# Optimization experiments

Hardware: AMD Instinct MI355X
Metric: run time of the kernel (lower is better)

Reference implementation:

```python
import jax, jax.numpy as jnp
import numpy as np

K = 1024          # num_embeddings
D = 768           # embedding_dim
COMMIT = 0.25     # commitment_cost
PW = 0.1          # perplexity_weight


def setup_inputs() -> dict:
    key = jax.random.key(0)
    k1, k2 = jax.random.split(key)
    inputs = jax.random.normal(k1, (32, 2048, D), dtype=jnp.float32)
    weight = jax.random.normal(k2, (K, D), dtype=jnp.float32)  # codebook
    return {"inputs": inputs, "weight": weight}


def reference(inputs, weight):
    """Eval-mode forward of VectorQuantizerEMA (deterministic nearest-code lookup)."""
    in_shape = inputs.shape
    flat = inputs.reshape(-1, D)                       # [N, D]
    valid = jnp.linalg.norm(flat, axis=1) > 1e-6       # padding mask [N]
    maskf = valid.astype(flat.dtype)
    n_valid = maskf.sum()

    dist = (jnp.sum(flat * flat, axis=1, keepdims=True)
            + jnp.sum(weight * weight, axis=1)
            - 2.0 * flat @ weight.T)

    idx = jnp.argmin(dist, axis=1)                     # [N]
    min_d = jnp.min(dist, axis=1)                      # [N]
    idx = jnp.where(valid, idx, 0)
    min_d = jnp.where(valid, min_d, 0.0)

    q_flat = weight[idx] * maskf[:, None]              # zeros at padded rows
    quantized = q_flat.reshape(in_shape)
    quantized_st = inputs + jax.lax.stop_gradient(quantized - inputs)

    # commitment loss: MSE over valid rows only
    sq_err = jnp.sum((flat - jax.lax.stop_gradient(q_flat)) ** 2, axis=1)
    loss_commit = jnp.sum(maskf * sq_err) / (n_valid * D)

    # perplexity over valid assignments (one-hot mean == normalized counts)
    counts = jnp.zeros((K,), flat.dtype).at[idx].add(maskf)
    avg_probs = counts / n_valid
    perplexity = jnp.exp(-jnp.sum(avg_probs * jnp.log(avg_probs + 1e-10)))
    perplexity_loss = -jnp.log(perplexity + 1e-10)

    total_loss = COMMIT * loss_commit + PW * perplexity_loss

    indices = idx.reshape(in_shape[:-1])
    min_distances = min_d.reshape(in_shape[:-1])
    return quantized_st, total_loss, indices, min_distances, perplexity
```

## Files before the change

kernel.cpp:

```cpp
#include <hip/hip_runtime.h>
#include <hip/hip_bf16.h>
#include <math.h>

#define NROWS 65536
#define DDIM  768
#define KCODES 1024
#define NCB   8
#define BM    128
#define BK    128
#define KC    32
#define NCH   (DDIM / KC)
#define BK2   32
#define NCH2  (DDIM / BK2)
#define GAP_TAU  0.3f
#define FILT_TAU 0.6f
#define RGRID 2048
#define QGRID 2048

#define OUT_LOSS ((size_t)NROWS * DDIM)
#define OUT_IDX  (OUT_LOSS + 1)
#define OUT_MIND (OUT_IDX + NROWS)
#define OUT_PERP (OUT_MIND + NROWS)

#define WS_SUM    0
#define WS_NSUS   8
#define WS_NVAL   12
#define WS_COUNTS 256
#define WS_WSQ    (WS_COUNTS + 4*KCODES)
#define WS_ROWS   (WS_WSQ + 4*KCODES)
#define WS_ROWI   (WS_ROWS + 4*NROWS)
#define WS_SUSP   (WS_ROWI + 4*NROWS)
#define WS_PM1    (WS_SUSP + 4*NROWS)
#define WS_PM2    (WS_PM1 + (size_t)4*NROWS*NCB)
#define WS_PIDX   (WS_PM2 + (size_t)4*NROWS*NCB)
#define WS_END    (WS_PIDX + (size_t)4*NROWS*NCB)
#define WS_AF16   ((WS_END + 255) & ~(size_t)255)
#define WS_WF16   (WS_AF16 + (size_t)NROWS * DDIM * 2)
#define WS_END2   (WS_WF16 + (size_t)KCODES * DDIM * 2)

typedef __attribute__((ext_vector_type(8))) _Float16 half8;
typedef __attribute__((ext_vector_type(4))) float f32x4;

#define GLOAD16(gsrc, ldst) \
    __builtin_amdgcn_global_load_lds( \
        (const __attribute__((address_space(1))) unsigned int*)(gsrc), \
        (__attribute__((address_space(3))) unsigned int*)(ldst), 16, 0, 0)

template <typename T>
__device__ inline T waveRedAdd(T v) {
#pragma unroll
    for (int o = 32; o; o >>= 1) v += __shfl_xor(v, o);
    return v;
}

__device__ inline ushort f2h(float f) {
    union { _Float16 h; ushort u; } c;
    c.h = (_Float16)f;
    return c.u;
}

__global__ void k_init(float* counts, int* n_suspect, unsigned* n_valid, double* sum_sqerr) {
    const int t = threadIdx.x;
    if (t == 0) { *n_suspect = 0; *n_valid = 0u; *sum_sqerr = 0.0; }
    for (int k = t; k < KCODES; k += 256) counts[k] = 0.f;
}

#define ASLOTS (NROWS * (DDIM / 8))
#define TSLOTS ((NROWS + KCODES) * (DDIM / 8))
__global__ __launch_bounds__(256) void k_convert(
    const float* __restrict__ A, const float* __restrict__ W,
    ushort* __restrict__ Af16, ushort* __restrict__ Wf16)
{
    for (int gidx = blockIdx.x * 256 + threadIdx.x; gidx < TSLOTS; gidx += gridDim.x * 256) {
        const float* src; ushort* dst; int sid;
        if (gidx < ASLOTS) { src = A; dst = Af16; sid = gidx; }
        else { src = W; dst = Wf16; sid = gidx - ASLOTS; }
        const int row = sid / 96;
        const int sl = sid - row * 96;
        const int ch = sl >> 2, s = sl & 3;
        const float* p = src + (size_t)row * DDIM + ch * 32 + s * 8;
        const float4 a = *(const float4*)p;
        const float4 b = *(const float4*)(p + 4);
        uint4 v;
        v.x = ((unsigned)f2h(a.y) << 16) | f2h(a.x);
        v.y = ((unsigned)f2h(a.w) << 16) | f2h(a.z);
        v.z = ((unsigned)f2h(b.y) << 16) | f2h(b.x);
        v.w = ((unsigned)f2h(b.w) << 16) | f2h(b.z);
        *(uint4*)(dst + (size_t)row * DDIM + ch * 32 + ((s ^ ((row >> 1) & 3)) << 3)) = v;
    }
}

__global__ __launch_bounds__(256) void k_wsq(const float* __restrict__ W, float* __restrict__ wsq) {
    const int k = blockIdx.x;
    const int t = threadIdx.x;
    const float* w = W + (size_t)k * DDIM;
    const float a = w[t], b = w[t + 256], c = w[t + 512];
    float s = a * a + b * b + c * c;
    s = waveRedAdd(s);
    __shared__ float p[4];
    if ((t & 63) == 0) p[t >> 6] = s;
    __syncthreads();
    if (t == 0) wsq[k] = (p[0] + p[1]) + (p[2] + p[3]);
}

__global__ __launch_bounds__(256, 4) void k_partials_g(
    const ushort* __restrict__ Af16, const ushort* __restrict__ Wf16,
    const float* __restrict__ wsq,
    float* __restrict__ pm1, float* __restrict__ pm2, int* __restrict__ pidx)
{
    __shared__ __align__(16) ushort lds[2 * 2 * BM * BK2];

    const int bid = blockIdx.x;
    const int rb = ((bid & 7) << 6) | (bid >> 6);
    const int cb = (bid >> 3) & 7;

    const int tid = threadIdx.x;
    const int wid = tid >> 6, lane = tid & 63;
    const int wr = wid >> 1, wc = wid & 1;
    const int l15 = lane & 15, g = lane >> 4;

    const ushort* Ab = Af16 + (size_t)rb * BM * DDIM;
    const ushort* Wb = Wf16 + (size_t)cb * BK * DDIM;

    const int srow = lane >> 2;
    const int sslot = lane & 3;

    f32x4 acc[4][4];
#pragma unroll
    for (int rt = 0; rt < 4; ++rt)
#pragma unroll
        for (int ct = 0; ct < 4; ++ct) acc[rt][ct] = (f32x4)0.f;

    auto STAGE = [&](int ch, int b) {
        ushort* As = lds + b * (2 * BM * BK2);
        ushort* Ws = As + BM * BK2;
#pragma unroll
        for (int i = 0; i < 2; ++i) {
            const int seg = (i << 2) | wid;
            const int row = (seg << 4) | srow;
            GLOAD16(Ab + (size_t)row * DDIM + ch * BK2 + sslot * 8, (char*)As + (seg << 10));
            GLOAD16(Wb + (size_t)row * DDIM + ch * BK2 + sslot * 8, (char*)Ws + (seg << 10));
        }
    };

    STAGE(0, 0);
    __syncthreads();

#pragma unroll 1
    for (int ch = 0; ch < NCH2; ++ch) {
        const int cur = ch & 1;
        if (ch + 1 < NCH2) STAGE(ch + 1, cur ^ 1);
        const ushort* As = lds + cur * (2 * BM * BK2);
        const ushort* Ws = As + BM * BK2;
        half8 bf[4];
#pragma unroll
        for (int ct = 0; ct < 4; ++ct) {
            const int c = wc * 64 + ct * 16 + l15;
            bf[ct] = *(const half8*)(Ws + c * BK2 + ((g ^ ((c >> 1) & 3)) << 3));
        }
#pragma unroll
        for (int rt = 0; rt < 4; ++rt) {
            const int r = wr * 64 + rt * 16 + l15;
            const half8 af = *(const half8*)(As + r * BK2 + ((g ^ ((r >> 1) & 3)) << 3));
#pragma unroll
            for (int ct = 0; ct < 4; ++ct)
                acc[rt][ct] = __builtin_amdgcn_mfma_f32_16x16x32_f16(af, bf[ct], acc[rt][ct], 0, 0, 0);
        }
        __syncthreads();
    }

    float wq[4];
#pragma unroll
    for (int ct = 0; ct < 4; ++ct) wq[ct] = wsq[cb * BK + wc * 64 + ct * 16 + l15];
    const int cbase = cb * BK + wc * 64 + l15;

    float* tm1 = (float*)lds;
    float* tm2 = tm1 + 256;
    int*   ti1 = (int*)(tm2 + 256);

#pragma unroll
    for (int rt = 0; rt < 4; ++rt) {
        float m1q[4], m2q[4]; int i1q[4];
#pragma unroll
        for (int q = 0; q < 4; ++q) { m1q[q] = INFINITY; m2q[q] = INFINITY; i1q[q] = 0x7fffffff; }
#pragma unroll
        for (int ct = 0; ct < 4; ++ct) {
            const int col = cbase + ct * 16;
#pragma unroll
            for (int q = 0; q < 4; ++q) {
                const float s = fmaf(-2.f, acc[rt][ct][q], wq[ct]);
                if (s < m1q[q]) { m2q[q] = m1q[q]; m1q[q] = s; i1q[q] = col; }
                else if (s < m2q[q]) m2q[q] = s;
            }
        }
#pragma unroll
        for (int msk = 1; msk <= 8; msk <<= 1) {
#pragma unroll
            for (int q = 0; q < 4; ++q) {
                const float om1 = __shfl_xor(m1q[q], msk);
                const float om2 = __shfl_xor(m2q[q], msk);
                const int   oi1 = __shfl_xor(i1q[q], msk);
                if (om1 < m1q[q] || (om1 == m1q[q] && oi1 < i1q[q])) {
                    m2q[q] = fminf(m1q[q], om2); m1q[q] = om1; i1q[q] = oi1;
                } else m2q[q] = fminf(m2q[q], om1);
            }
        }
        if (l15 == 0) {
#pragma unroll
            for (int q = 0; q < 4; ++q) {
                const int rl = wr * 64 + rt * 16 + g * 4 + q;
                tm1[rl * 2 + wc] = m1q[q];
                tm2[rl * 2 + wc] = m2q[q];
                ti1[rl * 2 + wc] = i1q[q];
            }
        }
    }
    __syncthreads();
    if (tid < BM) {
        float m1 = tm1[tid * 2], m2 = tm2[tid * 2]; int i1 = ti1[tid * 2];
        const float bm1 = tm1[tid * 2 + 1], bm2 = tm2[tid * 2 + 1]; const int bi = ti1[tid * 2 + 1];
        if (bm1 < m1 || (bm1 == m1 && bi < i1)) { m2 = fminf(m1, bm2); m1 = bm1; i1 = bi; }
        else m2 = fminf(m2, bm1);
        const size_t row = (size_t)rb * BM + tid;
        pm1[row * NCB + cb] = m1;
        pm2[row * NCB + cb] = m2;
        pidx[row * NCB + cb] = i1;
    }
}

__global__ __launch_bounds__(256, 2) void k_partials(
    const float* __restrict__ A, const float* __restrict__ W,
    const float* __restrict__ wsq,
    float* __restrict__ pm1, float* __restrict__ pm2, int* __restrict__ pidx)
{
    __shared__ __align__(16) ushort lds[2 * BM * KC];
    ushort* As = lds;
    ushort* Ws = lds + BM * KC;

    const int bid = blockIdx.x;
    const int rb = ((bid & 7) << 6) | (bid >> 6);
    const int cb = (bid >> 3) & 7;

    const int tid = threadIdx.x;
    const int wid = tid >> 6, lane = tid & 63;
    const int wr = wid >> 1, wc = wid & 1;
    const int l15 = lane & 15, g = lane >> 4;

    const float* Ab = A + (size_t)rb * BM * DDIM;
    const float* Wb = W + (size_t)cb * BK * DDIM;

    const int srow = tid >> 3;
    const int sk4  = (tid & 7) << 2;
    const int sg   = (tid & 7) >> 1;
    const int sh   = (tid & 1) << 2;

    int aOff[4], bOff[4];
#pragma unroll
    for (int rt = 0; rt < 4; ++rt) {
        const int r = wr * 64 + rt * 16 + l15;
        aOff[rt] = r * KC + ((g ^ ((r >> 1) & 3)) << 3);
        const int c = wc * 64 + rt * 16 + l15;
        bOff[rt] = c * KC + ((g ^ ((c >> 1) & 3)) << 3);
    }

    f32x4 acc[4][4];
#pragma unroll
    for (int rt = 0; rt < 4; ++rt)
#pragma unroll
        for (int ct = 0; ct < 4; ++ct) acc[rt][ct] = (f32x4)0.f;

    float4 av[4], wv[4];
#pragma unroll
    for (int i = 0; i < 4; ++i) {
        av[i] = *(const float4*)(Ab + (size_t)(srow + 32 * i) * DDIM + sk4);
        wv[i] = *(const float4*)(Wb + (size_t)(srow + 32 * i) * DDIM + sk4);
    }

#pragma unroll 1
    for (int ch = 0; ch < NCH; ++ch) {
        __syncthreads();
#pragma unroll
        for (int i = 0; i < 4; ++i) {
            const int r = srow + 32 * i;
            const int wsl = r * KC + ((sg ^ ((r >> 1) & 3)) << 3) + sh;
            ushort4 ua; ua.x = f2h(av[i].x); ua.y = f2h(av[i].y); ua.z = f2h(av[i].z); ua.w = f2h(av[i].w);
            *(ushort4*)(As + wsl) = ua;
            ushort4 uw; uw.x = f2h(wv[i].x); uw.y = f2h(wv[i].y); uw.z = f2h(wv[i].z); uw.w = f2h(wv[i].w);
            *(ushort4*)(Ws + wsl) = uw;
        }
        __syncthreads();
        if (ch + 1 < NCH) {
            const int d0 = (ch + 1) * KC + sk4;
#pragma unroll
            for (int i = 0; i < 4; ++i) {
                av[i] = *(const float4*)(Ab + (size_t)(srow + 32 * i) * DDIM + d0);
                wv[i] = *(const float4*)(Wb + (size_t)(srow + 32 * i) * DDIM + d0);
            }
        }
        half8 af[4], bf[4];
#pragma unroll
        for (int rt = 0; rt < 4; ++rt) af[rt] = *(const half8*)(As + aOff[rt]);
#pragma unroll
        for (int ct = 0; ct < 4; ++ct) bf[ct] = *(const half8*)(Ws + bOff[ct]);
#pragma unroll
        for (int rt = 0; rt < 4; ++rt)
#pragma unroll
            for (int ct = 0; ct < 4; ++ct)
                acc[rt][ct] = __builtin_amdgcn_mfma_f32_16x16x32_f16(af[rt], bf[ct], acc[rt][ct], 0, 0, 0);
    }

    float wq[4];
#pragma unroll
    for (int ct = 0; ct < 4; ++ct) wq[ct] = wsq[cb * BK + wc * 64 + ct * 16 + l15];
    const int cbase = cb * BK + wc * 64 + l15;

    __syncthreads();
    float* tm1 = (float*)lds;
    float* tm2 = tm1 + 256;
    int*   ti1 = (int*)(tm2 + 256);

#pragma unroll
    for (int rt = 0; rt < 4; ++rt) {
        float m1q[4], m2q[4]; int i1q[4];
#pragma unroll
        for (int q = 0; q < 4; ++q) { m1q[q] = INFINITY; m2q[q] = INFINITY; i1q[q] = 0x7fffffff; }
#pragma unroll
        for (int ct = 0; ct < 4; ++ct) {
            const int col = cbase + ct * 16;
#pragma unroll
            for (int q = 0; q < 4; ++q) {
                const float s = fmaf(-2.f, acc[rt][ct][q], wq[ct]);
                if (s < m1q[q]) { m2q[q] = m1q[q]; m1q[q] = s; i1q[q] = col; }
                else if (s < m2q[q]) m2q[q] = s;
            }
        }
#pragma unroll
        for (int msk = 1; msk <= 8; msk <<= 1) {
#pragma unroll
            for (int q = 0; q < 4; ++q) {
                const float om1 = __shfl_xor(m1q[q], msk);
                const float om2 = __shfl_xor(m2q[q], msk);
                const int   oi1 = __shfl_xor(i1q[q], msk);
                if (om1 < m1q[q] || (om1 == m1q[q] && oi1 < i1q[q])) {
                    m2q[q] = fminf(m1q[q], om2); m1q[q] = om1; i1q[q] = oi1;
                } else m2q[q] = fminf(m2q[q], om1);
            }
        }
        if (l15 == 0) {
#pragma unroll
            for (int q = 0; q < 4; ++q) {
                const int rl = wr * 64 + rt * 16 + g * 4 + q;
                tm1[rl * 2 + wc] = m1q[q];
                tm2[rl * 2 + wc] = m2q[q];
                ti1[rl * 2 + wc] = i1q[q];
            }
        }
    }
    __syncthreads();
    if (tid < BM) {
        float m1 = tm1[tid * 2], m2 = tm2[tid * 2]; int i1 = ti1[tid * 2];
        const float bm1 = tm1[tid * 2 + 1], bm2 = tm2[tid * 2 + 1]; const int bi = ti1[tid * 2 + 1];
        if (bm1 < m1 || (bm1 == m1 && bi < i1)) { m2 = fminf(m1, bm2); m1 = bm1; i1 = bi; }
        else m2 = fminf(m2, bm1);
        const size_t row = (size_t)rb * BM + tid;
        pm1[row * NCB + cb] = m1;
        pm2[row * NCB + cb] = m2;
        pidx[row * NCB + cb] = i1;
    }
}

__global__ __launch_bounds__(256) void k_merge(
    const float* __restrict__ pm1, const float* __restrict__ pm2, const int* __restrict__ pidx,
    float* __restrict__ row_s, int* __restrict__ row_idx,
    int* __restrict__ suspects, int* __restrict__ n_suspect)
{
    const int row = blockIdx.x * 256 + threadIdx.x;
    float m1 = INFINITY, m2 = INFINITY; int i1 = 0x7fffffff;
#pragma unroll
    for (int cb = 0; cb < NCB; ++cb) {
        const float bm1 = pm1[(size_t)row * NCB + cb];
        const float bm2 = pm2[(size_t)row * NCB + cb];
        const int   bi  = pidx[(size_t)row * NCB + cb];
        if (bm1 < m1 || (bm1 == m1 && bi < i1)) { m2 = fminf(m1, bm2); m1 = bm1; i1 = bi; }
        else m2 = fminf(m2, bm1);
    }
    row_s[row] = m1;
    row_idx[row] = i1;
    if (m2 - m1 < GAP_TAU) {
        const int p = atomicAdd(n_suspect, 1);
        suspects[p] = row;
    }
}

__global__ __launch_bounds__(256) void k_repair(
    const float* __restrict__ A, const float* __restrict__ W,
    const float* __restrict__ pm1,
    const int* __restrict__ suspects, const int* __restrict__ n_suspect,
    float* __restrict__ row_s, int* __restrict__ row_idx)
{
    __shared__ __align__(16) float xrow[DDIM];
    __shared__ double wbest[4]; __shared__ int wbi[4];
    __shared__ double xps[4];
    __shared__ int qcb[NCB];
    __shared__ int nq;
    const int ns = *n_suspect;
    const int tid = threadIdx.x;
    const int wid = tid >> 6, lane = tid & 63;
    const int sub = tid & 3;
    const int cq  = tid >> 2;

    for (int s = blockIdx.x; s < ns; s += gridDim.x) {
        const int row = suspects[s];
        __syncthreads();
        xrow[tid]       = A[(size_t)row * DDIM + tid];
        xrow[tid + 256] = A[(size_t)row * DDIM + tid + 256];
        xrow[tid + 512] = A[(size_t)row * DDIM + tid + 512];
        if (tid == 0) {
            float gmin = INFINITY;
#pragma unroll
            for (int cb = 0; cb < NCB; ++cb) gmin = fminf(gmin, pm1[(size_t)row * NCB + cb]);
            int n = 0;
#pragma unroll
            for (int cb = 0; cb < NCB; ++cb)
                if (pm1[(size_t)row * NCB + cb] <= gmin + FILT_TAU) qcb[n++] = cb;
            nq = n;
        }
        __syncthreads();

        double xp = 0.0;
        {
            double t;
            t = (double)xrow[tid];       xp = fma(t, t, xp);
            t = (double)xrow[tid + 256]; xp = fma(t, t, xp);
            t = (double)xrow[tid + 512]; xp = fma(t, t, xp);
        }
        xp = waveRedAdd(xp);
        if (lane == 0) xps[wid] = xp;

        double best = 1e300; int bi = 0x7fffffff;
        const int ncand = nq * BK;
        for (int base = 0; base < ncand; base += 64) {
            const int ci = base + cq;
            const bool act = ci < ncand;
            double d = 0.0; int k = 0x7fffffff;
            if (act) {
                k = qcb[ci >> 7] * BK + (ci & (BK - 1));
                const float* wr = W + (size_t)k * DDIM + (sub << 2);
                const float* xr = xrow + (sub << 2);
                double d0 = 0.0, d1 = 0.0;
                for (int i = 0; i < DDIM; i += 16) {
                    const float4 wv = *(const float4*)(wr + i);
                    const float4 xv = *(const float4*)(xr + i);
                    double t;
                    t = (double)xv.x - (double)wv.x; d0 = fma(t, t, d0);
                    t = (double)xv.y - (double)wv.y; d1 = fma(t, t, d1);
                    t = (double)xv.z - (double)wv.z; d0 = fma(t, t, d0);
                    t = (double)xv.w - (double)wv.w; d1 = fma(t, t, d1);
                }
                d = d0 + d1;
            }
            d += __shfl_xor(d, 1);
            d += __shfl_xor(d, 2);
            if (act && sub == 0) {
                if (d < best || (d == best && k < bi)) { best = d; bi = k; }
            }
        }
#pragma unroll
        for (int o = 32; o; o >>= 1) {
            const double ob = __shfl_xor(best, o);
            const int oi = __shfl_xor(bi, o);
            if (ob < best || (ob == best && oi < bi)) { best = ob; bi = oi; }
        }
        if (lane == 0) { wbest[wid] = best; wbi[wid] = bi; }
        __syncthreads();
        if (tid == 0) {
            double b = wbest[0]; int i1 = wbi[0];
#pragma unroll
            for (int w = 1; w < 4; ++w)
                if (wbest[w] < b || (wbest[w] == b && wbi[w] < i1)) { b = wbest[w]; i1 = wbi[w]; }
            row_idx[row] = i1;
            row_s[row] = (float)(b - (xps[0] + xps[1] + xps[2] + xps[3]));
        }
    }
}

__global__ __launch_bounds__(256) void k_quantize(
    const float* __restrict__ A, const float* __restrict__ W,
    const float* __restrict__ row_s, const int* __restrict__ row_idx,
    float* __restrict__ out, float* __restrict__ counts,
    unsigned int* __restrict__ n_valid, double* __restrict__ sum_sqerr)
{
    const int wid = threadIdx.x >> 6, lane = threadIdx.x & 63;
    __shared__ double s_sum[4];
    __shared__ unsigned s_val[4];
    double wsum = 0.0; unsigned wval = 0;

#pragma unroll 1
    for (int it = 0; it < NROWS / (QGRID * 4); ++it) {
        const int row = (it * QGRID + blockIdx.x) * 4 + wid;
        const float* x = A + (size_t)row * DDIM;
        float4 xv[3];
#pragma unroll
        for (int j = 0; j < 3; ++j) xv[j] = *(const float4*)(x + (lane + 64 * j) * 4);
        float xsq = 0.f;
#pragma unroll
        for (int j = 0; j < 3; ++j)
            xsq += xv[j].x * xv[j].x + xv[j].y * xv[j].y + xv[j].z * xv[j].z + xv[j].w * xv[j].w;
        xsq = waveRedAdd(xsq);
        const bool valid = xsq > 1e-12f;
        const float maskf = valid ? 1.f : 0.f;
        const int idx = row_idx[row];
        const int idxm = valid ? idx : 0;
        const float* w = W + (size_t)idx * DDIM;
        float* oq = out + (size_t)row * DDIM;
        float e2 = 0.f;
#pragma unroll
        for (int j = 0; j < 3; ++j) {
            const float4 wvv = *(const float4*)(w + (lane + 64 * j) * 4);
            const float xs[4] = {xv[j].x, xv[j].y, xv[j].z, xv[j].w};
            const float ws[4] = {wvv.x, wvv.y, wvv.z, wvv.w};
            float os[4];
#pragma unroll
            for (int c = 0; c < 4; ++c) {
                const float q = ws[c] * maskf;
                os[c] = xs[c] + (q - xs[c]);
                const float d = xs[c] - q;
                e2 += d * d;
            }
            float4 ov; ov.x = os[0]; ov.y = os[1]; ov.z = os[2]; ov.w = os[3];
            *(float4*)(oq + (lane + 64 * j) * 4) = ov;
        }
        e2 = waveRedAdd(e2);
        if (lane == 0) {
            wsum += (double)(maskf * e2);
            if (valid) {
                ++wval;
                atomicAdd(&counts[idxm], 1.0f);
            }
            out[OUT_IDX + row]  = (float)idxm;
            out[OUT_MIND + row] = valid ? (xsq + row_s[row]) : 0.f;
        }
    }

    if (lane == 0) { s_sum[wid] = wsum; s_val[wid] = wval; }
    __syncthreads();
    if (threadIdx.x == 0) {
        atomicAdd(sum_sqerr, s_sum[0] + s_sum[1] + s_sum[2] + s_sum[3]);
        atomicAdd(n_valid, s_val[0] + s_val[1] + s_val[2] + s_val[3]);
    }
}

__global__ __launch_bounds__(256) void k_final(
    const float* __restrict__ counts, const unsigned int* __restrict__ n_valid,
    const double* __restrict__ sum_sqerr, float* __restrict__ out)
{
    const int t = threadIdx.x;
    const float nv = (float)(*n_valid);
    double ent = 0.0;
    for (int k = t; k < KCODES; k += 256) {
        const float p = counts[k] / nv;
        ent += (double)(p * logf(p + 1e-10f));
    }
    ent = waveRedAdd(ent);
    __shared__ double ps[4];
    if ((t & 63) == 0) ps[t >> 6] = ent;
    __syncthreads();
    if (t == 0) {
        const double e = ps[0] + ps[1] + ps[2] + ps[3];
        const double perp = exp(-e);
        const double ploss = -log(perp + 1e-10);
        const double commit = *sum_sqerr / ((double)(*n_valid) * (double)DDIM);
        out[OUT_LOSS] = (float)(0.25 * commit + 0.1 * ploss);
        out[OUT_PERP] = (float)perp;
    }
}

extern "C" void kernel_launch(void* const* d_in, const int* in_sizes, int n_in,
                              void* d_out, int out_size, void* d_ws, size_t ws_size,
                              hipStream_t stream) {
    const float* A = (const float*)d_in[0];
    const float* W = (const float*)d_in[1];
    float* out = (float*)d_out;
    char* ws = (char*)d_ws;
    if (ws_size < (size_t)WS_END) return;

    double*   sum_sqerr = (double*)(ws + WS_SUM);
    int*      n_suspect = (int*)(ws + WS_NSUS);
    unsigned* n_valid   = (unsigned*)(ws + WS_NVAL);
    float*    counts    = (float*)(ws + WS_COUNTS);
    float*    wsq       = (float*)(ws + WS_WSQ);
    float*    row_s     = (float*)(ws + WS_ROWS);
    int*      row_idx   = (int*)(ws + WS_ROWI);
    int*      suspects  = (int*)(ws + WS_SUSP);
    float*    pm1       = (float*)(ws + WS_PM1);
    float*    pm2       = (float*)(ws + WS_PM2);
    int*      pidx      = (int*)(ws + WS_PIDX);
    ushort*   Af16      = (ushort*)(ws + WS_AF16);
    ushort*   Wf16      = (ushort*)(ws + WS_WF16);

    const bool big = ws_size >= (size_t)WS_END2;

    hipLaunchKernelGGL(k_init, dim3(1), dim3(256), 0, stream, counts, n_suspect, n_valid, sum_sqerr);
    if (big)
        hipLaunchKernelGGL(k_convert, dim3(2048), dim3(256), 0, stream, A, W, Af16, Wf16);
    hipLaunchKernelGGL(k_wsq, dim3(KCODES), dim3(256), 0, stream, W, wsq);
    if (big)
        hipLaunchKernelGGL(k_partials_g, dim3((NROWS / BM) * NCB), dim3(256), 0, stream, Af16, Wf16, wsq, pm1, pm2, pidx);
    else
        hipLaunchKernelGGL(k_partials, dim3((NROWS / BM) * NCB), dim3(256), 0, stream, A, W, wsq, pm1, pm2, pidx);
    hipLaunchKernelGGL(k_merge, dim3(NROWS / 256), dim3(256), 0, stream, pm1, pm2, pidx, row_s, row_idx, suspects, n_suspect);
    hipLaunchKernelGGL(k_repair, dim3(RGRID), dim3(256), 0, stream, A, W, pm1, suspects, n_suspect, row_s, row_idx);
    hipLaunchKernelGGL(k_quantize, dim3(QGRID), dim3(256), 0, stream, A, W, row_s, row_idx, out, counts, n_valid, sum_sqerr);
    hipLaunchKernelGGL(k_final, dim3(1), dim3(256), 0, stream, counts, n_valid, sum_sqerr, out);
}
```

Baseline: 368.0 us.

## Store fp16 operands in contiguous per-tile panels for linear GEMM staging loads

```diff
diff --git a/kernel.cpp b/kernel.cpp
--- a/kernel.cpp
+++ b/kernel.cpp
@@ -12,6 +12,7 @@
 #define NCH   (DDIM / KC)
 #define BK2   32
 #define NCH2  (DDIM / BK2)
+#define PANEL_USH (24 * 4096)
 #define GAP_TAU  0.3f
 #define FILT_TAU 0.6f
 #define RGRID 2048
@@ -86,7 +87,9 @@
         v.y = ((unsigned)f2h(a.w) << 16) | f2h(a.z);
         v.z = ((unsigned)f2h(b.y) << 16) | f2h(b.x);
         v.w = ((unsigned)f2h(b.w) << 16) | f2h(b.z);
-        *(uint4*)(dst + (size_t)row * DDIM + ch * 32 + ((s ^ ((row >> 1) & 3)) << 3)) = v;
+        const size_t dsti = (size_t)(row >> 7) * PANEL_USH + ch * 4096
+                          + (row & 127) * 32 + ((s ^ ((row >> 1) & 3)) << 3);
+        *(uint4*)(dst + dsti) = v;
     }
 }
 
@@ -119,11 +122,17 @@
     const int wr = wid >> 1, wc = wid & 1;
     const int l15 = lane & 15, g = lane >> 4;
 
-    const ushort* Ab = Af16 + (size_t)rb * BM * DDIM;
-    const ushort* Wb = Wf16 + (size_t)cb * BK * DDIM;
-
-    const int srow = lane >> 2;
-    const int sslot = lane & 3;
+    const ushort* Ap = Af16 + (size_t)rb * PANEL_USH;
+    const ushort* Wp = Wf16 + (size_t)cb * PANEL_USH;
+
+    int aoff[4], boff[4];
+#pragma unroll
+    for (int rt = 0; rt < 4; ++rt) {
+        const int r = wr * 64 + rt * 16 + l15;
+        aoff[rt] = r * 32 + ((g ^ ((r >> 1) & 3)) << 3);
+        const int c = wc * 64 + rt * 16 + l15;
+        boff[rt] = c * 32 + ((g ^ ((c >> 1) & 3)) << 3);
+    }
 
     f32x4 acc[4][4];
 #pragma unroll
@@ -131,37 +140,33 @@
 #pragma unroll
         for (int ct = 0; ct < 4; ++ct) acc[rt][ct] = (f32x4)0.f;
 
+    const int lseg = lane << 3;
     auto STAGE = [&](int ch, int b) {
-        ushort* As = lds + b * (2 * BM * BK2);
-        ushort* Ws = As + BM * BK2;
-#pragma unroll
-        for (int i = 0; i < 2; ++i) {
-            const int seg = (i << 2) | wid;
-            const int row = (seg << 4) | srow;
-            GLOAD16(Ab + (size_t)row * DDIM + ch * BK2 + sslot * 8, (char*)As + (seg << 10));
-            GLOAD16(Wb + (size_t)row * DDIM + ch * BK2 + sslot * 8, (char*)Ws + (seg << 10));
-        }
+        ushort* As = lds + b * 8192;
+        ushort* Ws = As + 4096;
+        const ushort* Asrc = Ap + ch * 4096;
+        const ushort* Wsrc = Wp + ch * 4096;
+        GLOAD16(Asrc + (wid << 9) + lseg,       (char*)As + (wid << 10));
+        GLOAD16(Asrc + ((wid + 4) << 9) + lseg, (char*)As + ((wid + 4) << 10));
+        GLOAD16(Wsrc + (wid << 9) + lseg,       (char*)Ws + (wid << 10));
+        GLOAD16(Wsrc + ((wid + 4) << 9) + lseg, (char*)Ws + ((wid + 4) << 10));
     };
 
     STAGE(0, 0);
     __syncthreads();
 
-#pragma unroll 1
+#pragma unroll 2
     for (int ch = 0; ch < NCH2; ++ch) {
         const int cur = ch & 1;
         if (ch + 1 < NCH2) STAGE(ch + 1, cur ^ 1);
-        const ushort* As = lds + cur * (2 * BM * BK2);
-        const ushort* Ws = As + BM * BK2;
+        const ushort* As = lds + cur * 8192;
+        const ushort* Ws = As + 4096;
         half8 bf[4];
 #pragma unroll
-        for (int ct = 0; ct < 4; ++ct) {
-            const int c = wc * 64 + ct * 16 + l15;
-            bf[ct] = *(const half8*)(Ws + c * BK2 + ((g ^ ((c >> 1) & 3)) << 3));
-        }
+        for (int ct = 0; ct < 4; ++ct) bf[ct] = *(const half8*)(Ws + boff[ct]);
 #pragma unroll
         for (int rt = 0; rt < 4; ++rt) {
-            const int r = wr * 64 + rt * 16 + l15;
-            const half8 af = *(const half8*)(As + r * BK2 + ((g ^ ((r >> 1) & 3)) << 3));
+            const half8 af = *(const half8*)(As + aoff[rt]);
 #pragma unroll
             for (int ct = 0; ct < 4; ++ct)
                 acc[rt][ct] = __builtin_amdgcn_mfma_f32_16x16x32_f16(af, bf[ct], acc[rt][ct], 0, 0, 0);
```

After: 364.9 us. No clear change (-0.8%).
